# Optimization experiments

Measured on AMD Instinct MI355X. Metric: run time of the kernel, lower is better.

The kernel has to match this reference:

```python
import jax, jax.numpy as jnp
import numpy as np

DIM = 1024
HEADS = 16
HEAD_DIM = DIM // HEADS
HIDDEN = 4 * DIM  # mlp_ratio = 4.0
EPS = 1e-5  # torch nn.LayerNorm default


def layernorm(x, gamma, beta):
    mu = jnp.mean(x, axis=-1, keepdims=True)
    var = jnp.mean(jnp.square(x - mu), axis=-1, keepdims=True)
    return (x - mu) * jax.lax.rsqrt(var + EPS) * gamma + beta


def setup_inputs() -> dict:
    key = jax.random.key(0)
    ks = jax.random.split(key, 12)
    s = lambda fan_in: 1.0 / np.sqrt(fan_in)
    return {
        "x": jax.random.normal(ks[0], (2, 2048, DIM), dtype=jnp.float32),
        "w_qkv": jax.random.normal(ks[1], (DIM, 3 * DIM), dtype=jnp.float32) * s(DIM),
        "b_qkv": jnp.zeros((3 * DIM,), dtype=jnp.float32),
        "w_proj": jax.random.normal(ks[2], (DIM, DIM), dtype=jnp.float32) * s(DIM),
        "b_proj": jnp.zeros((DIM,), dtype=jnp.float32),
        "g1": jnp.ones((DIM,), dtype=jnp.float32),
        "beta1": jnp.zeros((DIM,), dtype=jnp.float32),
        "g2": jnp.ones((DIM,), dtype=jnp.float32),
        "beta2": jnp.zeros((DIM,), dtype=jnp.float32),
        "w_fc1": jax.random.normal(ks[3], (DIM, HIDDEN), dtype=jnp.float32) * s(DIM),
        "b_fc1": jnp.zeros((HIDDEN,), dtype=jnp.float32),
        "w_fc2": jax.random.normal(ks[4], (HIDDEN, DIM), dtype=jnp.float32) * s(HIDDEN),
        "b_fc2": jnp.zeros((DIM,), dtype=jnp.float32),
    }


def reference(x, w_qkv, b_qkv, w_proj, b_proj, g1, beta1, g2, beta2,
              w_fc1, b_fc1, w_fc2, b_fc2):
    B, S, D = x.shape
    # --- attention branch: norm1 -> qkv -> causal MHA -> proj -> residual ---
    h = layernorm(x, g1, beta1)
    qkv = h @ w_qkv + b_qkv                      # [B, S, 3D]
    qkv = qkv.reshape(B, S, 3, HEADS, HEAD_DIM)
    q, k, v = qkv[:, :, 0], qkv[:, :, 1], qkv[:, :, 2]  # [B, S, H, d]
    scale = 1.0 / np.sqrt(HEAD_DIM)
    scores = jnp.einsum("bqhd,bkhd->bhqk", q, k) * scale  # [B, H, S, S]
    causal = jnp.tril(jnp.ones((S, S), dtype=bool))
    scores = jnp.where(causal, scores, jnp.finfo(scores.dtype).min)
    attn = jax.nn.softmax(scores, axis=-1)
    out = jnp.einsum("bhqk,bkhd->bqhd", attn, v).reshape(B, S, D)
    x = x + (out @ w_proj + b_proj)
    # --- ffn residual branch: norm2 -> fc1 -> GELU -> fc2 -> residual ---
    h = layernorm(x, g2, beta2)
    h = jax.nn.gelu(h @ w_fc1 + b_fc1, approximate=False)
    x = x + (h @ w_fc2 + b_fc2)
    return x
```

## Files before the change

kernel.cpp:

```cpp
#include <hip/hip_runtime.h>

typedef unsigned short u16;
typedef unsigned int u32;
typedef short s16x8 __attribute__((ext_vector_type(8)));
typedef short s16x4 __attribute__((ext_vector_type(4)));
typedef float f32x4 __attribute__((ext_vector_type(4)));

__device__ __forceinline__ u16 f2b(float f){
  union { float f; unsigned int i; } v; v.f = f;
  unsigned int r = v.i + 0x7FFFu + ((v.i >> 16) & 1u);
  return (u16)(r >> 16);
}
__device__ __forceinline__ u32 asu(float f){
  union { float f; unsigned int i; } v; v.f = f; return v.i;
}
__device__ __forceinline__ u32 pkbf(float a, float b){
  return __builtin_amdgcn_perm(asu(b) + 0x8000u, asu(a) + 0x8000u, 0x07060302u);
}

__device__ __forceinline__ void gl_lds16(const u16* g, u16* l) {
  __builtin_amdgcn_global_load_lds(
    (const __attribute__((address_space(1))) unsigned int*)(g),
    (__attribute__((address_space(3))) unsigned int*)(l), 16, 0, 0);
}

__global__ __launch_bounds__(256) void transpose_k(const float* __restrict__ in,
                                                   u16* __restrict__ out, int K, int N)
{
  __shared__ u16 tile[32][33];
  const int tx = threadIdx.x, ty = threadIdx.y;
  const int x = blockIdx.x * 32 + tx;
  const int y0 = blockIdx.y * 32;
  #pragma unroll
  for (int j = ty; j < 32; j += 8)
    tile[j][tx] = f2b(in[(size_t)(y0 + j) * N + x]);
  __syncthreads();
  const int x2 = y0 + tx;
  const int y2 = blockIdx.x * 32;
  #pragma unroll
  for (int j = ty; j < 32; j += 8)
    out[(size_t)(y2 + j) * K + x2] = tile[tx][j];
}

__global__ __launch_bounds__(256) void ln_k(const float* __restrict__ xin,
                                            const float* __restrict__ g,
                                            const float* __restrict__ be,
                                            u16* __restrict__ out)
{
  const int row = blockIdx.x, tid = threadIdx.x;
  float4 u = *(const float4*)(xin + (size_t)row * 1024 + tid * 4);
  float v[4] = {u.x, u.y, u.z, u.w};
  float sum = v[0] + v[1] + v[2] + v[3];
  float sq  = v[0]*v[0] + v[1]*v[1] + v[2]*v[2] + v[3]*v[3];
  #pragma unroll
  for (int off = 32; off > 0; off >>= 1) {
    sum += __shfl_down(sum, off, 64);
    sq  += __shfl_down(sq,  off, 64);
  }
  __shared__ float ws1[4], ws2[4];
  const int wid = tid >> 6, lane = tid & 63;
  if (lane == 0) { ws1[wid] = sum; ws2[wid] = sq; }
  __syncthreads();
  const float tot  = ws1[0] + ws1[1] + ws1[2] + ws1[3];
  const float tot2 = ws2[0] + ws2[1] + ws2[2] + ws2[3];
  const float inv = 1.0f / 1024.0f;
  const float mu = tot * inv;
  const float var = tot2 * inv - mu * mu;
  const float rs = rsqrtf(var + 1e-5f);
  float4 gv = *(const float4*)(g  + tid * 4);
  float4 bv = *(const float4*)(be + tid * 4);
  u16 ob[4];
  ob[0] = f2b((v[0] - mu) * rs * gv.x + bv.x);
  ob[1] = f2b((v[1] - mu) * rs * gv.y + bv.y);
  ob[2] = f2b((v[2] - mu) * rs * gv.z + bv.z);
  ob[3] = f2b((v[3] - mu) * rs * gv.w + bv.w);
  uint2 o;
  o.x = (unsigned)ob[0] | ((unsigned)ob[1] << 16);
  o.y = (unsigned)ob[2] | ((unsigned)ob[3] << 16);
  *(uint2*)(out + (size_t)row * 1024 + tid * 4) = o;
}

template<int ACT, bool RES, bool OUTF>
__global__ __launch_bounds__(256) void gemm_lds(const u16* __restrict__ A, int lda,
                                                const u16* __restrict__ Bt, int ldb,
                                                const float* __restrict__ bias,
                                                const float* __restrict__ res,
                                                void* __restrict__ Cout,
                                                int K, int ldc)
{
  __shared__ __align__(16) u16 As[128 * 64];
  __shared__ __align__(16) u16 Bs[128 * 64];
  const int tid = threadIdx.x;
  const int wid = tid >> 6, lane = tid & 63, quad = lane >> 4, ln = lane & 15;
  const int wr = wid >> 1, wc = wid & 1;
  const int m0 = blockIdx.y * 128, n0 = blockIdx.x * 128;

  f32x4 acc[4][4];
  #pragma unroll
  for (int i = 0; i < 4; ++i)
    #pragma unroll
    for (int j = 0; j < 4; ++j)
      #pragma unroll
      for (int r = 0; r < 4; ++r) acc[i][j][r] = 0.f;

  const int srow = wid * 32 + (lane >> 3);
  const int scol = (((lane & 7) ^ (lane >> 3)) & 7) * 8;

  for (int k0 = 0; k0 < K; k0 += 64) {
    __syncthreads();
    #pragma unroll
    for (int i = 0; i < 4; ++i) {
      const int row = srow + i * 8;
      gl_lds16(&A [(size_t)(m0 + row) * lda + k0 + scol], &As[wid * 2048 + i * 512]);
      gl_lds16(&Bt[(size_t)(n0 + row) * ldb + k0 + scol], &Bs[wid * 2048 + i * 512]);
    }
    __syncthreads();
    #pragma unroll
    for (int ks = 0; ks < 2; ++ks) {
      const int cgx = (((4*ks + quad) ^ (ln & 7)) & 7) * 8;
      s16x8 af[4], bfr[4];
      #pragma unroll
      for (int i = 0; i < 4; ++i) af[i]  = *(const s16x8*)&As[(wr*64 + i*16 + ln)*64 + cgx];
      #pragma unroll
      for (int j = 0; j < 4; ++j) bfr[j] = *(const s16x8*)&Bs[(wc*64 + j*16 + ln)*64 + cgx];
      #pragma unroll
      for (int i = 0; i < 4; ++i)
        #pragma unroll
        for (int j = 0; j < 4; ++j)
          acc[i][j] = __builtin_amdgcn_mfma_f32_16x16x32_bf16(af[i], bfr[j], acc[i][j], 0, 0, 0);
    }
  }
  float bv[4];
  #pragma unroll
  for (int j = 0; j < 4; ++j) bv[j] = bias ? bias[n0 + wc*64 + j*16 + ln] : 0.f;
  #pragma unroll
  for (int i = 0; i < 4; ++i) {
    #pragma unroll
    for (int r = 0; r < 4; ++r) {
      const int row = m0 + wr*64 + i*16 + quad*4 + r;
      #pragma unroll
      for (int j = 0; j < 4; ++j) {
        const int col = n0 + wc*64 + j*16 + ln;
        const size_t idx = (size_t)row * ldc + col;
        float v = acc[i][j][r] + bv[j];
        if (RES) v += res[idx];
        if (ACT == 1) v = 0.5f * v * (1.f + erff(v * 0.70710678118f));
        if (OUTF) ((float*)Cout)[idx] = v;
        else      ((u16*)Cout)[idx] = f2b(v);
      }
    }
  }
}

template<int ACT, bool RES, bool OUTF>
__global__ __launch_bounds__(512) void gemm_pf2(const u16* __restrict__ A, int lda,
                                                const u16* __restrict__ Bt, int ldb,
                                                const float* __restrict__ bias,
                                                const float* __restrict__ res,
                                                void* __restrict__ Cout,
                                                int K, int ldc)
{
  constexpr int LDP = 72;
  __shared__ __align__(16) u16 As[2][128 * LDP];
  __shared__ __align__(16) u16 Bs[2][128 * LDP];
  const int tid = threadIdx.x;
  const int wid = tid >> 6, lane = tid & 63, quad = lane >> 4, ln = lane & 15;
  const int wr = wid >> 1, wc = wid & 1;
  const int m0 = blockIdx.x * 128, n0 = blockIdx.y * 128;

  f32x4 acc[2][4];
  #pragma unroll
  for (int i = 0; i < 2; ++i)
    #pragma unroll
    for (int j = 0; j < 4; ++j)
      #pragma unroll
      for (int r = 0; r < 4; ++r) acc[i][j][r] = 0.f;

  const int lr = tid >> 2;
  const int lc = (tid & 3) * 16;
  const u16* Ab = &A [(size_t)(m0 + lr) * lda + lc];
  const u16* Bb = &Bt[(size_t)(n0 + lr) * ldb + lc];

  s16x8 ra[2], rb[2];
  ra[0] = *(const s16x8*)(Ab);     ra[1] = *(const s16x8*)(Ab + 8);
  rb[0] = *(const s16x8*)(Bb);     rb[1] = *(const s16x8*)(Bb + 8);
  *(s16x8*)&As[0][lr*LDP + lc]     = ra[0];
  *(s16x8*)&As[0][lr*LDP + lc + 8] = ra[1];
  *(s16x8*)&Bs[0][lr*LDP + lc]     = rb[0];
  *(s16x8*)&Bs[0][lr*LDP + lc + 8] = rb[1];
  const int nk = K >> 6;
  if (nk > 1) {
    ra[0] = *(const s16x8*)(Ab + 64);  ra[1] = *(const s16x8*)(Ab + 72);
    rb[0] = *(const s16x8*)(Bb + 64);  rb[1] = *(const s16x8*)(Bb + 72);
  }
  __syncthreads();

  for (int k = 0; k < nk; ++k) {
    if (k + 1 < nk) {
      const int p = (k + 1) & 1;
      *(s16x8*)&As[p][lr*LDP + lc]     = ra[0];
      *(s16x8*)&As[p][lr*LDP + lc + 8] = ra[1];
      *(s16x8*)&Bs[p][lr*LDP + lc]     = rb[0];
      *(s16x8*)&Bs[p][lr*LDP + lc + 8] = rb[1];
      if (k + 2 < nk) {
        const u16* An = Ab + (k + 2) * 64;
        const u16* Bn = Bb + (k + 2) * 64;
        ra[0] = *(const s16x8*)(An);  ra[1] = *(const s16x8*)(An + 8);
        rb[0] = *(const s16x8*)(Bn);  rb[1] = *(const s16x8*)(Bn + 8);
      }
    }
    const int c = k & 1;
    #pragma unroll
    for (int ks = 0; ks < 2; ++ks) {
      s16x8 af[2], bfr[4];
      #pragma unroll
      for (int i = 0; i < 2; ++i) af[i]  = *(const s16x8*)&As[c][(wr*32 + i*16 + ln)*LDP + ks*32 + quad*8];
      #pragma unroll
      for (int j = 0; j < 4; ++j) bfr[j] = *(const s16x8*)&Bs[c][(wc*64 + j*16 + ln)*LDP + ks*32 + quad*8];
      #pragma unroll
      for (int i = 0; i < 2; ++i)
        #pragma unroll
        for (int j = 0; j < 4; ++j)
          acc[i][j] = __builtin_amdgcn_mfma_f32_16x16x32_bf16(af[i], bfr[j], acc[i][j], 0, 0, 0);
    }
    __syncthreads();
  }

  float bv[4];
  #pragma unroll
  for (int j = 0; j < 4; ++j) bv[j] = bias ? bias[n0 + wc*64 + j*16 + ln] : 0.f;
  #pragma unroll
  for (int i = 0; i < 2; ++i) {
    #pragma unroll
    for (int r = 0; r < 4; ++r) {
      const int row = m0 + wr*32 + i*16 + quad*4 + r;
      #pragma unroll
      for (int j = 0; j < 4; ++j) {
        const int col = n0 + wc*64 + j*16 + ln;
        const size_t idx = (size_t)row * ldc + col;
        float v = acc[i][j][r] + bv[j];
        if (RES) v += res[idx];
        if (ACT == 1) v = 0.5f * v * (1.f + erff(v * 0.70710678118f));
        if (OUTF) ((float*)Cout)[idx] = v;
        else      ((u16*)Cout)[idx] = f2b(v);
      }
    }
  }
}

__global__ __launch_bounds__(256) void attn_k(const u16* __restrict__ qkv,
                                              u16* __restrict__ outp)
{
  constexpr int LDK = 72;
  __shared__ __align__(16) u16 Kt[64 * LDK];
  __shared__ __align__(16) u16 Vt[64 * LDK];
  const int tid = threadIdx.x, wid = tid >> 6, lane = tid & 63;
  const int quad = lane >> 4, ln = lane & 15;
  const int qb = 31 - (blockIdx.x >> 5);
  const int bh = blockIdx.x & 31, b = bh >> 4, h = bh & 15;
  const u16* base = qkv + (size_t)b * 2048 * 3072;
  const float C = 0.18033688f;

  const int tkr = tid >> 2, tkc = (tid & 3) * 16;
  const int qln = qb * 64 + wid * 16 + ln;

  s16x8 aQ0, aQ1;
  {
    const u16* qrow = base + (size_t)qln * 3072 + h * 64 + quad * 8;
    aQ0 = *(const s16x8*)(qrow);
    aQ1 = *(const s16x8*)(qrow + 32);
  }
  f32x4 o[4];
  float lsum = 0.f;
  #pragma unroll
  for (int dt = 0; dt < 4; ++dt)
    #pragma unroll
    for (int r = 0; r < 4; ++r) o[dt][r] = 0.f;

  for (int kt = 0; kt < qb; ++kt) {
    const int kb = kt * 64;
    __syncthreads();
    {
      const u16* krow = base + (size_t)(kb + tkr) * 3072 + 1024 + h * 64 + tkc;
      *(s16x8*)&Kt[tkr * LDK + tkc]     = *(const s16x8*)(krow);
      *(s16x8*)&Kt[tkr * LDK + tkc + 8] = *(const s16x8*)(krow + 8);
      const u16* vrow = base + (size_t)(kb + lane) * 3072 + 2048 + h * 64 + wid * 16;
      s16x8 va = *(const s16x8*)(vrow);
      s16x8 vb = *(const s16x8*)(vrow + 8);
      #pragma unroll
      for (int e = 0; e < 8; ++e) {
        Vt[(wid * 16 + e) * LDK + lane]     = (u16)va[e];
        Vt[(wid * 16 + 8 + e) * LDK + lane] = (u16)vb[e];
      }
    }
    __syncthreads();

    #pragma unroll
    for (int mt = 0; mt < 4; ++mt) {
      f32x4 s;
      #pragma unroll
      for (int r = 0; r < 4; ++r) s[r] = 0.f;
      s16x8 k0 = *(const s16x8*)&Kt[(mt*16 + ln) * LDK + quad * 8];
      s16x8 k1 = *(const s16x8*)&Kt[(mt*16 + ln) * LDK + 32 + quad * 8];
      s = __builtin_amdgcn_mfma_f32_16x16x32_bf16(k0, aQ0, s, 0, 0, 0);
      s = __builtin_amdgcn_mfma_f32_16x16x32_bf16(k1, aQ1, s, 0, 0, 0);
      float p0 = exp2f(s[0] * C), p1 = exp2f(s[1] * C);
      float p2 = exp2f(s[2] * C), p3 = exp2f(s[3] * C);
      lsum += (p0 + p1) + (p2 + p3);
      union { u32 u[2]; s16x4 v; } bp;
      bp.u[0] = pkbf(p0, p1); bp.u[1] = pkbf(p2, p3);
      #pragma unroll
      for (int dt = 0; dt < 4; ++dt) {
        s16x4 aV = *(const s16x4*)&Vt[(dt*16 + ln) * LDK + mt*16 + quad*4];
        o[dt] = __builtin_amdgcn_mfma_f32_16x16x16bf16_1k(aV, bp.v, o[dt], 0, 0, 0);
      }
    }
  }

  {
    const int kb = qb * 64;
    __syncthreads();
    {
      const u16* krow = base + (size_t)(kb + tkr) * 3072 + 1024 + h * 64 + tkc;
      *(s16x8*)&Kt[tkr * LDK + tkc]     = *(const s16x8*)(krow);
      *(s16x8*)&Kt[tkr * LDK + tkc + 8] = *(const s16x8*)(krow + 8);
      const u16* vrow = base + (size_t)(kb + lane) * 3072 + 2048 + h * 64 + wid * 16;
      s16x8 va = *(const s16x8*)(vrow);
      s16x8 vb = *(const s16x8*)(vrow + 8);
      #pragma unroll
      for (int e = 0; e < 8; ++e) {
        Vt[(wid * 16 + e) * LDK + lane]     = (u16)va[e];
        Vt[(wid * 16 + 8 + e) * LDK + lane] = (u16)vb[e];
      }
    }
    __syncthreads();

    #pragma unroll
    for (int mt = 0; mt < 4; ++mt) {
      if (mt <= wid) {
        f32x4 s;
        #pragma unroll
        for (int r = 0; r < 4; ++r) s[r] = 0.f;
        s16x8 k0 = *(const s16x8*)&Kt[(mt*16 + ln) * LDK + quad * 8];
        s16x8 k1 = *(const s16x8*)&Kt[(mt*16 + ln) * LDK + 32 + quad * 8];
        s = __builtin_amdgcn_mfma_f32_16x16x32_bf16(k0, aQ0, s, 0, 0, 0);
        s = __builtin_amdgcn_mfma_f32_16x16x32_bf16(k1, aQ1, s, 0, 0, 0);
        float p[4];
        #pragma unroll
        for (int r = 0; r < 4; ++r) {
          p[r] = exp2f(s[r] * C);
          if (mt == wid && (quad*4 + r) > ln) p[r] = 0.f;
        }
        lsum += (p[0] + p[1]) + (p[2] + p[3]);
        union { u32 u[2]; s16x4 v; } bp;
        bp.u[0] = pkbf(p[0], p[1]); bp.u[1] = pkbf(p[2], p[3]);
        #pragma unroll
        for (int dt = 0; dt < 4; ++dt) {
          s16x4 aV = *(const s16x4*)&Vt[(dt*16 + ln) * LDK + mt*16 + quad*4];
          o[dt] = __builtin_amdgcn_mfma_f32_16x16x16bf16_1k(aV, bp.v, o[dt], 0, 0, 0);
        }
      }
    }
  }

  lsum += __shfl_xor(lsum, 16, 64);
  lsum += __shfl_xor(lsum, 32, 64);
  const float inv = 1.0f / lsum;

  u16* orow = outp + (size_t)(b * 2048 + qln) * 1024 + h * 64;
  #pragma unroll
  for (int dt = 0; dt < 4; ++dt) {
    uint2 w;
    w.x = pkbf(o[dt][0] * inv, o[dt][1] * inv);
    w.y = pkbf(o[dt][2] * inv, o[dt][3] * inv);
    *(uint2*)(orow + dt*16 + quad*4) = w;
  }
}

extern "C" void kernel_launch(void* const* d_in, const int* in_sizes, int n_in,
                              void* d_out, int out_size, void* d_ws, size_t ws_size,
                              hipStream_t stream)
{
  (void)in_sizes; (void)n_in; (void)out_size;
  const float* x      = (const float*)d_in[0];
  const float* w_qkv  = (const float*)d_in[1];
  const float* b_qkv  = (const float*)d_in[2];
  const float* w_proj = (const float*)d_in[3];
  const float* b_proj = (const float*)d_in[4];
  const float* g1     = (const float*)d_in[5];
  const float* be1    = (const float*)d_in[6];
  const float* g2     = (const float*)d_in[7];
  const float* be2    = (const float*)d_in[8];
  const float* w_fc1  = (const float*)d_in[9];
  const float* b_fc1  = (const float*)d_in[10];
  const float* w_fc2  = (const float*)d_in[11];
  const float* b_fc2  = (const float*)d_in[12];

  u16* base    = (u16*)d_ws;
  u16* hbuf    = base;
  u16* wt_qkv  = base + (size_t) 4194304;
  u16* wt_proj = base + (size_t) 7340032;
  u16* qkvb    = base + (size_t) 8388608;
  float* x2f   = (float*)(base + (size_t)8388608);
  u16* wt_fc2  = base + (size_t)16777216;
  u16* wt_fc1  = base + (size_t) 4194304;
  u16* fbuf    = base + (size_t)20971520;
  u16* attnb   = (u16*)d_out;
  float* outf  = (float*)d_out;

  dim3 tb(32, 8);

  ln_k<<<4096, 256, 0, stream>>>(x, g1, be1, hbuf);
  transpose_k<<<dim3(96, 32), tb, 0, stream>>>(w_qkv, wt_qkv, 1024, 3072);
  gemm_lds<0,false,false><<<dim3(24, 32), 256, 0, stream>>>(hbuf, 1024, wt_qkv, 1024,
                                                            b_qkv, nullptr, qkvb, 1024, 3072);
  attn_k<<<1024, 256, 0, stream>>>(qkvb, attnb);

  transpose_k<<<dim3(32, 128), tb, 0, stream>>>(w_fc2, wt_fc2, 4096, 1024);
  transpose_k<<<dim3(32, 32),  tb, 0, stream>>>(w_proj, wt_proj, 1024, 1024);
  gemm_pf2<0,true,true><<<dim3(32, 8), 512, 0, stream>>>(attnb, 1024, wt_proj, 1024,
                                                         b_proj, x, x2f, 1024, 1024);
  transpose_k<<<dim3(128, 32), tb, 0, stream>>>(w_fc1, wt_fc1, 1024, 4096);
  ln_k<<<4096, 256, 0, stream>>>(x2f, g2, be2, hbuf);

  if (ws_size >= (size_t)72 * 1024 * 1024) {
    gemm_lds<1,false,false><<<dim3(32, 32), 256, 0, stream>>>(hbuf, 1024, wt_fc1, 1024,
                                                              b_fc1, nullptr, fbuf, 1024, 4096);
    gemm_pf2<0,true,true><<<dim3(32, 8), 512, 0, stream>>>(fbuf, 4096, wt_fc2, 4096,
                                                           b_fc2, x2f, outf, 4096, 1024);
  } else {
    gemm_lds<1,false,false><<<dim3(16, 32), 256, 0, stream>>>(hbuf, 1024, wt_fc1, 1024,
                                                              b_fc1, nullptr, fbuf, 1024, 2048);
    gemm_pf2<0,true,true><<<dim3(32, 8), 512, 0, stream>>>(fbuf, 2048, wt_fc2, 4096,
                                                           b_fc2, x2f, x2f, 2048, 1024);
    gemm_lds<1,false,false><<<dim3(16, 32), 256, 0, stream>>>(hbuf, 1024,
                                                              wt_fc1 + (size_t)2048*1024, 1024,
                                                              b_fc1 + 2048, nullptr, fbuf, 1024, 2048);
    gemm_pf2<0,true,true><<<dim3(32, 8), 512, 0, stream>>>(fbuf, 2048, wt_fc2 + 2048, 4096,
                                                           nullptr, x2f, outf, 2048, 1024);
  }
}
```

Measured before the change: 393.2 us.

## Pre-transpose V, use direct global-to-LDS loads with XOR swizzle in attention and GEMM

Adds a kernel that transposes V into a per-head [d, S] buffer so the attention kernel can fill its K and V tiles with direct global_load_lds 16-byte copies. This replaces the per-element scalar LDS scatter used for V. The LDS tiles in attention and in gemm_pf2 drop the 72-element row padding in favour of an XOR swizzle, which avoids bank conflicts while shrinking LDS use. The diagonal tile is merged into the main loop. The trade-off is an extra launch plus a full V transpose pass through global memory, stored in a workspace region reused later by fbuf.

```diff
diff --git a/kernel.cpp b/kernel.cpp
--- a/kernel.cpp
+++ b/kernel.cpp
@@ -40,6 +40,23 @@
   #pragma unroll
   for (int j = ty; j < 32; j += 8)
     out[(size_t)(y2 + j) * K + x2] = tile[tx][j];
+}
+
+__global__ __launch_bounds__(256) void vt_k(const u16* __restrict__ qkv,
+                                            u16* __restrict__ vtg)
+{
+  __shared__ u16 tile[32][33];
+  const int bh = blockIdx.z, b = bh >> 4, h = bh & 15;
+  const int x0 = blockIdx.x * 32;
+  const int y0 = blockIdx.y * 32;
+  const int tx = threadIdx.x, ty = threadIdx.y;
+  #pragma unroll
+  for (int j = ty; j < 32; j += 8)
+    tile[j][tx] = qkv[(size_t)(b * 2048 + y0 + j) * 3072 + 2048 + h * 64 + x0 + tx];
+  __syncthreads();
+  #pragma unroll
+  for (int j = ty; j < 32; j += 8)
+    vtg[((size_t)bh * 64 + x0 + j) * 2048 + y0 + tx] = tile[tx][j];
 }
 
 __global__ __launch_bounds__(256) void ln_k(const float* __restrict__ xin,
@@ -160,9 +177,8 @@
                                                 void* __restrict__ Cout,
                                                 int K, int ldc)
 {
-  constexpr int LDP = 72;
-  __shared__ __align__(16) u16 As[2][128 * LDP];
-  __shared__ __align__(16) u16 Bs[2][128 * LDP];
+  __shared__ __align__(16) u16 As[2][128 * 64];
+  __shared__ __align__(16) u16 Bs[2][128 * 64];
   const int tid = threadIdx.x;
   const int wid = tid >> 6, lane = tid & 63, quad = lane >> 4, ln = lane & 15;
   const int wr = wid >> 1, wc = wid & 1;
@@ -178,16 +194,18 @@
 
   const int lr = tid >> 2;
   const int lc = (tid & 3) * 16;
+  const int s1 = (((tid & 3) * 2)     ^ (lr & 7)) * 8;
+  const int s2 = (((tid & 3) * 2 + 1) ^ (lr & 7)) * 8;
   const u16* Ab = &A [(size_t)(m0 + lr) * lda + lc];
   const u16* Bb = &Bt[(size_t)(n0 + lr) * ldb + lc];
 
   s16x8 ra[2], rb[2];
   ra[0] = *(const s16x8*)(Ab);     ra[1] = *(const s16x8*)(Ab + 8);
   rb[0] = *(const s16x8*)(Bb);     rb[1] = *(const s16x8*)(Bb + 8);
-  *(s16x8*)&As[0][lr*LDP + lc]     = ra[0];
-  *(s16x8*)&As[0][lr*LDP + lc + 8] = ra[1];
-  *(s16x8*)&Bs[0][lr*LDP + lc]     = rb[0];
-  *(s16x8*)&Bs[0][lr*LDP + lc + 8] = rb[1];
+  *(s16x8*)&As[0][lr*64 + s1] = ra[0];
+  *(s16x8*)&As[0][lr*64 + s2] = ra[1];
+  *(s16x8*)&Bs[0][lr*64 + s1] = rb[0];
+  *(s16x8*)&Bs[0][lr*64 + s2] = rb[1];
   const int nk = K >> 6;
   if (nk > 1) {
     ra[0] = *(const s16x8*)(Ab + 64);  ra[1] = *(const s16x8*)(Ab + 72);
@@ -198,10 +216,10 @@
   for (int k = 0; k < nk; ++k) {
     if (k + 1 < nk) {
       const int p = (k + 1) & 1;
-      *(s16x8*)&As[p][lr*LDP + lc]     = ra[0];
-      *(s16x8*)&As[p][lr*LDP + lc + 8] = ra[1];
-      *(s16x8*)&Bs[p][lr*LDP + lc]     = rb[0];
-      *(s16x8*)&Bs[p][lr*LDP + lc + 8] = rb[1];
+      *(s16x8*)&As[p][lr*64 + s1] = ra[0];
+      *(s16x8*)&As[p][lr*64 + s2] = ra[1];
+      *(s16x8*)&Bs[p][lr*64 + s1] = rb[0];
+      *(s16x8*)&Bs[p][lr*64 + s2] = rb[1];
       if (k + 2 < nk) {
         const u16* An = Ab + (k + 2) * 64;
         const u16* Bn = Bb + (k + 2) * 64;
@@ -212,11 +230,12 @@
     const int c = k & 1;
     #pragma unroll
     for (int ks = 0; ks < 2; ++ks) {
+      const int cgx = (((4*ks + quad) ^ (ln & 7)) & 7) * 8;
       s16x8 af[2], bfr[4];
       #pragma unroll
-      for (int i = 0; i < 2; ++i) af[i]  = *(const s16x8*)&As[c][(wr*32 + i*16 + ln)*LDP + ks*32 + quad*8];
-      #pragma unroll
-      for (int j = 0; j < 4; ++j) bfr[j] = *(const s16x8*)&Bs[c][(wc*64 + j*16 + ln)*LDP + ks*32 + quad*8];
+      for (int i = 0; i < 2; ++i) af[i]  = *(const s16x8*)&As[c][(wr*32 + i*16 + ln)*64 + cgx];
+      #pragma unroll
+      for (int j = 0; j < 4; ++j) bfr[j] = *(const s16x8*)&Bs[c][(wc*64 + j*16 + ln)*64 + cgx];
       #pragma unroll
       for (int i = 0; i < 2; ++i)
         #pragma unroll
@@ -249,19 +268,21 @@
 }
 
 __global__ __launch_bounds__(256) void attn_k(const u16* __restrict__ qkv,
+                                              const u16* __restrict__ vtg,
                                               u16* __restrict__ outp)
 {
-  constexpr int LDK = 72;
-  __shared__ __align__(16) u16 Kt[64 * LDK];
-  __shared__ __align__(16) u16 Vt[64 * LDK];
+  __shared__ __align__(16) u16 Kt[64 * 64];
+  __shared__ __align__(16) u16 Vt[64 * 64];
   const int tid = threadIdx.x, wid = tid >> 6, lane = tid & 63;
   const int quad = lane >> 4, ln = lane & 15;
   const int qb = 31 - (blockIdx.x >> 5);
   const int bh = blockIdx.x & 31, b = bh >> 4, h = bh & 15;
   const u16* base = qkv + (size_t)b * 2048 * 3072;
+  const u16* vbase = vtg + (size_t)bh * 64 * 2048;
   const float C = 0.18033688f;
 
-  const int tkr = tid >> 2, tkc = (tid & 3) * 16;
+  const int grow = (lane >> 3);
+  const int gch  = ((lane & 7) ^ (lane >> 3)) * 8;
   const int qln = qb * 64 + wid * 16 + ln;
 
   s16x8 aQ0, aQ1;
@@ -277,88 +298,43 @@
     #pragma unroll
     for (int r = 0; r < 4; ++r) o[dt][r] = 0.f;
 
-  for (int kt = 0; kt < qb; ++kt) {
+  const int nkt = qb + 1;
+  for (int kt = 0; kt < nkt; ++kt) {
     const int kb = kt * 64;
     __syncthreads();
-    {
-      const u16* krow = base + (size_t)(kb + tkr) * 3072 + 1024 + h * 64 + tkc;
-      *(s16x8*)&Kt[tkr * LDK + tkc]     = *(const s16x8*)(krow);
-      *(s16x8*)&Kt[tkr * LDK + tkc + 8] = *(const s16x8*)(krow + 8);
-      const u16* vrow = base + (size_t)(kb + lane) * 3072 + 2048 + h * 64 + wid * 16;
-      s16x8 va = *(const s16x8*)(vrow);
-      s16x8 vb = *(const s16x8*)(vrow + 8);
-      #pragma unroll
-      for (int e = 0; e < 8; ++e) {
-        Vt[(wid * 16 + e) * LDK + lane]     = (u16)va[e];
-        Vt[(wid * 16 + 8 + e) * LDK + lane] = (u16)vb[e];
-      }
+    #pragma unroll
+    for (int i = 0; i < 2; ++i) {
+      const int r = wid * 16 + i * 8 + grow;
+      gl_lds16(base  + (size_t)(kb + r) * 3072 + 1024 + h * 64 + gch, &Kt[wid * 1024 + i * 512]);
+      gl_lds16(vbase + (size_t)r * 2048 + kb + gch,                   &Vt[wid * 1024 + i * 512]);
     }
     __syncthreads();
 
-    #pragma unroll
-    for (int mt = 0; mt < 4; ++mt) {
+    const int mtn = (kt < qb) ? 4 : (wid + 1);
+    for (int mt = 0; mt < mtn; ++mt) {
       f32x4 s;
       #pragma unroll
       for (int r = 0; r < 4; ++r) s[r] = 0.f;
-      s16x8 k0 = *(const s16x8*)&Kt[(mt*16 + ln) * LDK + quad * 8];
-      s16x8 k1 = *(const s16x8*)&Kt[(mt*16 + ln) * LDK + 32 + quad * 8];
+      const int krow = (mt*16 + ln) * 64;
+      s16x8 k0 = *(const s16x8*)&Kt[krow + ((quad     ^ (ln & 7)) * 8)];
+      s16x8 k1 = *(const s16x8*)&Kt[krow + (((4+quad) ^ (ln & 7)) * 8)];
       s = __builtin_amdgcn_mfma_f32_16x16x32_bf16(k0, aQ0, s, 0, 0, 0);
       s = __builtin_amdgcn_mfma_f32_16x16x32_bf16(k1, aQ1, s, 0, 0, 0);
-      float p0 = exp2f(s[0] * C), p1 = exp2f(s[1] * C);
-      float p2 = exp2f(s[2] * C), p3 = exp2f(s[3] * C);
-      lsum += (p0 + p1) + (p2 + p3);
+      float p[4];
+      #pragma unroll
+      for (int r = 0; r < 4; ++r) p[r] = exp2f(s[r] * C);
+      if (kt == qb && mt == wid) {
+        #pragma unroll
+        for (int r = 0; r < 4; ++r) if ((quad*4 + r) > ln) p[r] = 0.f;
+      }
+      lsum += (p[0] + p[1]) + (p[2] + p[3]);
       union { u32 u[2]; s16x4 v; } bp;
-      bp.u[0] = pkbf(p0, p1); bp.u[1] = pkbf(p2, p3);
+      bp.u[0] = pkbf(p[0], p[1]); bp.u[1] = pkbf(p[2], p[3]);
+      const int vch = ((2*mt + (quad >> 1)) ^ (ln & 7)) * 8 + (quad & 1) * 4;
       #pragma unroll
       for (int dt = 0; dt < 4; ++dt) {
-        s16x4 aV = *(const s16x4*)&Vt[(dt*16 + ln) * LDK + mt*16 + quad*4];
+        s16x4 aV = *(const s16x4*)&Vt[(dt*16 + ln) * 64 + vch];
         o[dt] = __builtin_amdgcn_mfma_f32_16x16x16bf16_1k(aV, bp.v, o[dt], 0, 0, 0);
-      }
-    }
-  }
-
-  {
-    const int kb = qb * 64;
-    __syncthreads();
-    {
-      const u16* krow = base + (size_t)(kb + tkr) * 3072 + 1024 + h * 64 + tkc;
-      *(s16x8*)&Kt[tkr * LDK + tkc]     = *(const s16x8*)(krow);
-      *(s16x8*)&Kt[tkr * LDK + tkc + 8] = *(const s16x8*)(krow + 8);
-      const u16* vrow = base + (size_t)(kb + lane) * 3072 + 2048 + h * 64 + wid * 16;
-      s16x8 va = *(const s16x8*)(vrow);
-      s16x8 vb = *(const s16x8*)(vrow + 8);
-      #pragma unroll
-      for (int e = 0; e < 8; ++e) {
-        Vt[(wid * 16 + e) * LDK + lane]     = (u16)va[e];
-        Vt[(wid * 16 + 8 + e) * LDK + lane] = (u16)vb[e];
-      }
-    }
-    __syncthreads();
-
-    #pragma unroll
-    for (int mt = 0; mt < 4; ++mt) {
-      if (mt <= wid) {
-        f32x4 s;
-        #pragma unroll
-        for (int r = 0; r < 4; ++r) s[r] = 0.f;
-        s16x8 k0 = *(const s16x8*)&Kt[(mt*16 + ln) * LDK + quad * 8];
-        s16x8 k1 = *(const s16x8*)&Kt[(mt*16 + ln) * LDK + 32 + quad * 8];
-        s = __builtin_amdgcn_mfma_f32_16x16x32_bf16(k0, aQ0, s, 0, 0, 0);
-        s = __builtin_amdgcn_mfma_f32_16x16x32_bf16(k1, aQ1, s, 0, 0, 0);
-        float p[4];
-        #pragma unroll
-        for (int r = 0; r < 4; ++r) {
-          p[r] = exp2f(s[r] * C);
-          if (mt == wid && (quad*4 + r) > ln) p[r] = 0.f;
-        }
-        lsum += (p[0] + p[1]) + (p[2] + p[3]);
-        union { u32 u[2]; s16x4 v; } bp;
-        bp.u[0] = pkbf(p[0], p[1]); bp.u[1] = pkbf(p[2], p[3]);
-        #pragma unroll
-        for (int dt = 0; dt < 4; ++dt) {
-          s16x4 aV = *(const s16x4*)&Vt[(dt*16 + ln) * LDK + mt*16 + quad*4];
-          o[dt] = __builtin_amdgcn_mfma_f32_16x16x16bf16_1k(aV, bp.v, o[dt], 0, 0, 0);
-        }
       }
     }
   }
@@ -404,6 +380,7 @@
   float* x2f   = (float*)(base + (size_t)8388608);
   u16* wt_fc2  = base + (size_t)16777216;
   u16* wt_fc1  = base + (size_t) 4194304;
+  u16* vtg     = base + (size_t)20971520;
   u16* fbuf    = base + (size_t)20971520;
   u16* attnb   = (u16*)d_out;
   float* outf  = (float*)d_out;
@@ -414,7 +391,8 @@
   transpose_k<<<dim3(96, 32), tb, 0, stream>>>(w_qkv, wt_qkv, 1024, 3072);
   gemm_lds<0,false,false><<<dim3(24, 32), 256, 0, stream>>>(hbuf, 1024, wt_qkv, 1024,
                                                             b_qkv, nullptr, qkvb, 1024, 3072);
-  attn_k<<<1024, 256, 0, stream>>>(qkvb, attnb);
+  vt_k<<<dim3(2, 64, 32), tb, 0, stream>>>(qkvb, vtg);
+  attn_k<<<1024, 256, 0, stream>>>(qkvb, vtg, attnb);
 
   transpose_k<<<dim3(32, 128), tb, 0, stream>>>(w_fc2, wt_fc2, 4096, 1024);
   transpose_k<<<dim3(32, 32),  tb, 0, stream>>>(w_proj, wt_proj, 1024, 1024);
```

Result: faster. 357.3 us (-9.1%).
